# Kernel optimization log

Measured on AMD Instinct MI355X. Metric: run time of the kernel, lower is better.

## Reference

```python
import jax, jax.numpy as jnp
import numpy as np

KX, KZ = 3, 3          # heterogeneity_x, heterogeneity_z
DX, DZ, DU = 3, 3, 3   # depths
LX, LZ = 16, 16        # last_x, last_z
TOL = 1e-6


def setup_inputs() -> dict:
    key = jax.random.key(0)
    ks = jax.random.split(key, 11)
    B, n, dx, dz = 8192, 50, 32, 20
    WXw, WZw, WUw = 64, 64, 128

    def w(k, shape):
        return jax.random.normal(k, shape, jnp.float32) * (1.0 / np.sqrt(shape[-2]))

    return {
        "X": jax.random.normal(ks[0], (B, n, dx), jnp.float32),
        "Z": jax.random.normal(ks[1], (B, dz), jnp.float32),
        "Wx0": w(ks[2], (KX, dx, WXw)),
        "Wx": w(ks[3], (KX, DX - 1, WXw, WXw)),
        "Wlx": w(ks[4], (KX, WXw, LX)),
        "Wz0": w(ks[5], (KZ, dz, WZw)),
        "Wz": w(ks[6], (KZ, DZ - 1, WZw, WZw)),
        "Wlz": w(ks[7], (KZ, WZw, LZ)),
        "Wu0": w(ks[8], (dx + LX + LZ + dz, WUw)),
        "Wu": w(ks[9], (DU - 1, WUw, WUw)),
        "Wlast": w(ks[10], (WUw, 1)),
    }


def reference(X, Z, Wx0, Wx, Wlx, Wz0, Wz, Wlz, Wu0, Wu, Wlast):
    B, n, dx = X.shape
    dz = Z.shape[-1]

    # --- product-feature MLP per heterogeneity i, batched over all n products ---
    # NOTE (faithful to original bug): the leaked loop var `k` means
    # last_x[DX-1] is used for EVERY heterogeneity index i.
    def x_branch(w0, wh):
        h = jax.nn.elu(jnp.einsum('bnd,dw->bnw', X, w0))
        for k in range(wh.shape[0]):
            h = jax.nn.elu(jnp.einsum('bnw,wv->bnv', h, wh[k]))
        return jnp.einsum('bnw,wl->bnl', h, Wlx[DX - 1])  # linear last layer

    Xi = jax.vmap(x_branch)(Wx0, Wx)  # [KX, B, n, LX]

    # --- customer-feature MLP per heterogeneity j ---
    def z_branch(w0, wh, wl):
        h = jax.nn.elu(Z @ w0)
        for k in range(wh.shape[0]):
            h = jax.nn.elu(h @ wh[k])
        return h @ wl  # linear last layer

    Zj = jax.vmap(z_branch)(Wz0, Wz, Wlz)  # [KZ, B, LZ]

    # --- utility MLP over all (i, j) heterogeneity pairs; average of softmaxes ---
    acc = jnp.zeros((B, n), X.dtype)
    for i in range(KX):
        for j in range(KZ):
            zb = jnp.broadcast_to(Zj[j][:, None, :], (B, n, LZ))
            zu = jnp.broadcast_to(Z[:, None, :], (B, n, dz))
            u = jnp.concatenate([X, Xi[i], zb, zu], axis=-1)  # [B, n, dx+LX+LZ+dz]
            u = jax.nn.elu(u @ Wu0)
            for k in range(Wu.shape[0]):
                u = jax.nn.elu(u @ Wu[k])
            score = (u @ Wlast)[..., 0]  # [B, n]
            acc = acc + (TOL + jax.nn.softmax(score, axis=-1)) / (1.0 + TOL * n)
    return acc / (KX * KZ)
```

## Files before the change

### kernel.cpp

```cpp
#include <hip/hip_runtime.h>
#include <math.h>

#define NPROD 50
#define DXF 32
#define DZF 20
#define WUW 128
#define LXD 16
#define LZD 16

typedef __attribute__((ext_vector_type(8))) short short8;
typedef __attribute__((ext_vector_type(4))) float float4_;

__device__ __forceinline__ short f2bf(float x) {
    unsigned u = __builtin_bit_cast(unsigned, x);
    u += 0x7fffu + ((u >> 16) & 1u);
    return (short)(u >> 16);
}
__device__ __forceinline__ unsigned pkbf(float a, float b) {
#if __has_builtin(__builtin_amdgcn_cvt_pk_bf16_f32)
    auto v = __builtin_amdgcn_cvt_pk_bf16_f32(a, b);
    return __builtin_bit_cast(unsigned, v);
#else
    return (unsigned)(unsigned short)f2bf(a) | ((unsigned)(unsigned short)f2bf(b) << 16);
#endif
}
__device__ __forceinline__ float elu_med3(float x) {
    float e = __builtin_amdgcn_exp2f(x * 1.44269504089f) - 1.0f;
#if __has_builtin(__builtin_amdgcn_fmed3f)
    return __builtin_amdgcn_fmed3f(x, e, 0.0f);
#else
    return x > 0.0f ? x : e;
#endif
}
__device__ __forceinline__ float elu_fast(float x) {
    float e = __builtin_amdgcn_exp2f(x * 1.44269504089f) - 1.0f;
    return x > 0.0f ? x : e;
}
#define MFMA16(a, b, c) __builtin_amdgcn_mfma_f32_16x16x32_bf16((a), (b), (c), 0, 0, 0)

#define PK_WX0   0
#define PK_WX    6144
#define PK_WLX2  30720
#define PK_WU0   31744
#define PK_WU    39936
#define PK_WLAST 72704
#define PK_TOTAL 74752
#define NB_PACK  292
#define WS_NEEDED ((size_t)PK_TOTAL * 2)

__device__ __forceinline__ short* su_ptr(short* buf, int row, int chunk) {
    return buf + (row << 7) + ((chunk ^ (row & 15)) << 3);
}
__device__ __forceinline__ const short* su_ptr(const short* buf, int row, int chunk) {
    return buf + (row << 7) + ((chunk ^ (row & 15)) << 3);
}
__device__ __forceinline__ short* sa_ptr(short* buf, int row, int chunk) {
    return buf + (row << 6) + ((chunk ^ (row & 7)) << 3);
}
__device__ __forceinline__ const short* sa_ptr(const short* buf, int row, int chunk) {
    return buf + (row << 6) + ((chunk ^ (row & 7)) << 3);
}

template<bool ACT>
__device__ __forceinline__ void epi_store(short* chunk_base, int half, float4_ a) {
    float e0, e1, e2, e3;
    if (ACT) { e0 = elu_med3(a[0]); e1 = elu_med3(a[1]); e2 = elu_med3(a[2]); e3 = elu_med3(a[3]); }
    else { e0 = a[0]; e1 = a[1]; e2 = a[2]; e3 = a[3]; }
    uint2 p; p.x = pkbf(e0, e1); p.y = pkbf(e2, e3);
    *(uint2*)(chunk_base + half * 4) = p;
}

__global__ void pack_weights(const float* __restrict__ Wx0, const float* __restrict__ Wx,
                             const float* __restrict__ Wlx, const float* __restrict__ Wu0,
                             const float* __restrict__ Wu, const float* __restrict__ Wlast,
                             short* __restrict__ pk)
{
    int idx = blockIdx.x * 256 + threadIdx.x;
    if (idx >= PK_TOTAL) return;
    float v;
    if (idx < PK_WX) {
        int m = idx / 2048, r = idx % 2048, n = r / 32, k = r % 32;
        v = Wx0[m * 2048 + k * 64 + n];
    } else if (idx < PK_WLX2) {
        int t = idx - PK_WX; int m = t / 4096, r = t % 4096, n = r / 64, k = r % 64;
        v = Wx[m * 4096 + k * 64 + n];
    } else if (idx < PK_WU0) {
        int r = idx - PK_WLX2; int n = r / 64, k = r % 64;
        v = Wlx[2 * 1024 + k * 16 + n];
    } else if (idx < PK_WU) {
        int r = idx - PK_WU0; int n = r / 64, k = r % 64;
        v = (k < 48) ? Wu0[k * 128 + n] : 0.0f;
    } else if (idx < PK_WLAST) {
        int t = idx - PK_WU; int m = t / 16384, r = t % 16384, n = r / 128, k = r % 128;
        v = Wu[m * 16384 + k * 128 + n];
    } else {
        int r = idx - PK_WLAST; int n = r / 128, k = r % 128;
        v = (n == 0) ? Wlast[k] : 0.0f;
    }
    pk[idx] = f2bf(v);
}

__global__ __launch_bounds__(256, 3) void rum_main(
    const float* __restrict__ X, const float* __restrict__ Z,
    const float* __restrict__ Wz0, const float* __restrict__ Wz,
    const float* __restrict__ Wlz, const float* __restrict__ Wu0,
    const short* __restrict__ pk, float* __restrict__ out)
{
    __shared__ __align__(16) short sA0[64 * 64];
    __shared__ __align__(16) short sU[64 * 128];
    __shared__ __align__(16) float sPreZ[3 * 128];
    __shared__ float sScore[2][64];
    __shared__ float sZb[DZF];
    __shared__ float zA[3][64], zB[3][64];
    __shared__ float sZj[3][LZD];

    const int tid = threadIdx.x;
    const int w = tid >> 6, lane = tid & 63;
    const int quad = lane >> 4, l15 = lane & 15;
    const long b = blockIdx.x;
    const short8 zero8 = (short8)0;

    for (int it = tid; it < 100; it += 256) {
        int r = it >> 1, ch = 6 + (it & 1);
        *(short8*)sa_ptr(sA0, r, ch) = zero8;
    }
    if (tid < 112) {
        int r = 50 + (tid >> 3), ch = tid & 7;
        *(short8*)sa_ptr(sA0, r, ch) = zero8;
    }
    for (int it = tid; it < 400; it += 256) {
        int r = it >> 3, c4 = it & 7;
        float4_ xv = *(const float4_*)(X + (b * 50 + r) * 32 + c4 * 4);
        uint2 p; p.x = pkbf(xv[0], xv[1]); p.y = pkbf(xv[2], xv[3]);
        *(uint2*)(sa_ptr(sA0, r, c4 >> 1) + (c4 & 1) * 4) = p;
    }
    if (tid < DZF) sZb[tid] = Z[b * DZF + tid];
    __syncthreads();

    if (w < 3) {
        const float* wv = Wz0 + w * (DZF * 64);
        float s0 = 0.f, s1 = 0.f;
        #pragma unroll
        for (int k = 0; k < DZF; k += 2) {
            s0 = fmaf(sZb[k], wv[k * 64 + lane], s0);
            s1 = fmaf(sZb[k + 1], wv[(k + 1) * 64 + lane], s1);
        }
        zA[w][lane] = elu_fast(s0 + s1);
    }
    __syncthreads();
    if (w < 3) {
        const float* wv = Wz + (w * 2 + 0) * 4096;
        float s0 = 0.f, s1 = 0.f;
        #pragma unroll
        for (int k = 0; k < 64; k += 2) {
            s0 = fmaf(zA[w][k], wv[k * 64 + lane], s0);
            s1 = fmaf(zA[w][k + 1], wv[(k + 1) * 64 + lane], s1);
        }
        zB[w][lane] = elu_fast(s0 + s1);
    }
    __syncthreads();
    if (w < 3) {
        const float* wv = Wz + (w * 2 + 1) * 4096;
        float s0 = 0.f, s1 = 0.f;
        #pragma unroll
        for (int k = 0; k < 64; k += 2) {
            s0 = fmaf(zB[w][k], wv[k * 64 + lane], s0);
            s1 = fmaf(zB[w][k + 1], wv[(k + 1) * 64 + lane], s1);
        }
        zA[w][lane] = elu_fast(s0 + s1);
    }
    __syncthreads();
    if (w < 3 && lane < LZD) {
        const float* wv = Wlz + w * (64 * LZD);
        float s0 = 0.f, s1 = 0.f;
        #pragma unroll
        for (int k = 0; k < 64; k += 2) {
            s0 = fmaf(zA[w][k], wv[k * LZD + lane], s0);
            s1 = fmaf(zA[w][k + 1], wv[(k + 1) * LZD + lane], s1);
        }
        sZj[w][lane] = s0 + s1;
    }
    __syncthreads();
    if (w < 3) {
        #pragma unroll
        for (int half = 0; half < 2; ++half) {
            const int c = lane + half * 64;
            float s = 0.f;
            #pragma unroll
            for (int k = 0; k < LZD; ++k) s = fmaf(sZj[w][k], Wu0[(48 + k) * WUW + c], s);
            #pragma unroll
            for (int k = 0; k < DZF; ++k) s = fmaf(sZb[k], Wu0[(64 + k) * WUW + c], s);
            sPreZ[w * 128 + c] = s;
        }
    }
    __syncthreads();

    float accv = 0.f;
    const float inv_norm = 1.0f / (1.0f + 1e-6f * (float)NPROD);

    for (int i = 0; i < 3; ++i) {
        {
            const short* A = pk + PK_WX0 + i * 2048;
            short8 af = *(const short8*)(A + (w * 16 + l15) * 32 + quad * 8);
            #pragma unroll
            for (int pt = 0; pt < 4; ++pt) {
                short8 bfr = *(const short8*)sa_ptr(sA0, pt * 16 + l15, quad);
                float4_ acc = MFMA16(af, bfr, (float4_)0.f);
                epi_store<true>(su_ptr(sU, pt * 16 + l15, 2 * w + (quad >> 1)), quad & 1, acc);
            }
        }
        __syncthreads();
        for (int l = 0; l < 2; ++l) {
            const short* A = pk + PK_WX + (i * 2 + l) * 4096;
            short8 af0 = *(const short8*)(A + (w * 16 + l15) * 64 + quad * 8);
            short8 af1 = *(const short8*)(A + (w * 16 + l15) * 64 + 32 + quad * 8);
            float4_ accx[4];
            #pragma unroll
            for (int pt = 0; pt < 4; ++pt) {
                short8 b0 = *(const short8*)su_ptr(sU, pt * 16 + l15, quad);
                short8 b1 = *(const short8*)su_ptr(sU, pt * 16 + l15, 4 + quad);
                accx[pt] = MFMA16(af0, b0, (float4_)0.f);
                accx[pt] = MFMA16(af1, b1, accx[pt]);
            }
            __syncthreads();
            #pragma unroll
            for (int pt = 0; pt < 4; ++pt)
                epi_store<true>(su_ptr(sU, pt * 16 + l15, 2 * w + (quad >> 1)), quad & 1, accx[pt]);
            __syncthreads();
        }
        {
            const short* A = pk + PK_WLX2;
            short8 af0 = *(const short8*)(A + l15 * 64 + quad * 8);
            short8 af1 = *(const short8*)(A + l15 * 64 + 32 + quad * 8);
            short8 b0 = *(const short8*)su_ptr(sU, w * 16 + l15, quad);
            short8 b1 = *(const short8*)su_ptr(sU, w * 16 + l15, 4 + quad);
            float4_ acc = MFMA16(af0, b0, (float4_)0.f);
            acc = MFMA16(af1, b1, acc);
            epi_store<false>(sa_ptr(sA0, w * 16 + l15, 4 + (quad >> 1)), quad & 1, acc);
        }
        __syncthreads();

        for (int j = 0; j < 3; ++j) {
            const int pass = i * 3 + j;
            {
                const short* A = pk + PK_WU0;
                #pragma unroll
                for (int wi = 0; wi < 2; ++wi) {
                    const int wt = w * 2 + wi;
                    float4_ pz = *(const float4_*)(sPreZ + j * 128 + wt * 16 + quad * 4);
                    short8 af0 = *(const short8*)(A + (wt * 16 + l15) * 64 + quad * 8);
                    short8 af1 = *(const short8*)(A + (wt * 16 + l15) * 64 + 32 + quad * 8);
                    #pragma unroll
                    for (int pt = 0; pt < 4; ++pt) {
                        short8 b0 = *(const short8*)sa_ptr(sA0, pt * 16 + l15, quad);
                        short8 b1 = *(const short8*)sa_ptr(sA0, pt * 16 + l15, 4 + quad);
                        float4_ t = MFMA16(af0, b0, pz);
                        t = MFMA16(af1, b1, t);
                        epi_store<true>(su_ptr(sU, pt * 16 + l15, 2 * wt + (quad >> 1)), quad & 1, t);
                    }
                }
            }
            __syncthreads();

            for (int l = 0; l < 2; ++l) {
                const short* A = pk + PK_WU + l * 16384;
                float4_ ad[2][4];
                #pragma unroll
                for (int wi = 0; wi < 2; ++wi)
                    #pragma unroll
                    for (int pt = 0; pt < 4; ++pt) ad[wi][pt] = (float4_)0.f;
                #pragma unroll
                for (int ks = 0; ks < 4; ++ks) {
                    short8 bf[4];
                    #pragma unroll
                    for (int pt = 0; pt < 4; ++pt)
                        bf[pt] = *(const short8*)su_ptr(sU, pt * 16 + l15, ks * 4 + quad);
                    #pragma unroll
                    for (int wi = 0; wi < 2; ++wi) {
                        short8 af = *(const short8*)(A + ((w * 2 + wi) * 16 + l15) * 128 + ks * 32 + quad * 8);
                        #pragma unroll
                        for (int pt = 0; pt < 4; ++pt)
                            ad[wi][pt] = MFMA16(af, bf[pt], ad[wi][pt]);
                    }
                }
                __syncthreads();
                #pragma unroll
                for (int wi = 0; wi < 2; ++wi)
                    #pragma unroll
                    for (int pt = 0; pt < 4; ++pt)
                        epi_store<true>(su_ptr(sU, pt * 16 + l15, 2 * (w * 2 + wi) + (quad >> 1)),
                                        quad & 1, ad[wi][pt]);
                __syncthreads();
            }

            {
                const short* A = pk + PK_WLAST;
                float4_ as = (float4_)0.f;
                #pragma unroll
                for (int ks = 0; ks < 4; ++ks) {
                    short8 af = *(const short8*)(A + l15 * 128 + ks * 32 + quad * 8);
                    short8 bf = *(const short8*)su_ptr(sU, w * 16 + l15, ks * 4 + quad);
                    as = MFMA16(af, bf, as);
                }
                if (quad == 0) sScore[pass & 1][w * 16 + l15] = as[0];
            }
            __syncthreads();
            if (tid < 64) {
                float sc = (tid < NPROD) ? sScore[pass & 1][tid] : -3.0e38f;
                float m = sc;
                #pragma unroll
                for (int off = 32; off > 0; off >>= 1) m = fmaxf(m, __shfl_xor(m, off));
                float e = (tid < NPROD) ? __builtin_amdgcn_exp2f((sc - m) * 1.44269504089f) : 0.f;
                float ssum = e;
                #pragma unroll
                for (int off = 32; off > 0; off >>= 1) ssum += __shfl_xor(ssum, off);
                if (tid < NPROD) accv += (1e-6f + e / ssum) * inv_norm;
            }
        }
    }
    if (tid < NPROD) out[b * 50 + tid] = accv * (1.0f / 9.0f);
}

__device__ __forceinline__ float elu_f(float x) { return x > 0.0f ? x : expm1f(x); }
template<int IN, int OUT, bool ACT>
__device__ __forceinline__ void dense50(const float* __restrict__ in_lds,
                                        const float* __restrict__ Wg,
                                        float* __restrict__ out_lds)
{
    const int tid = threadIdx.x;
    constexpr int CQ = OUT / 4;
    const float4* __restrict__ W4 = (const float4*)Wg;
    for (int item = tid; item < 25 * CQ; item += 256) {
        const int rp = item / CQ, cq = item % CQ;
        const int r0 = rp, r1 = rp + 25;
        float4 a0 = {0,0,0,0}, a1 = {0,0,0,0};
        for (int k = 0; k < IN; ++k) {
            const float4 wv = W4[k * CQ + cq];
            const float x0 = in_lds[r0 * IN + k], x1 = in_lds[r1 * IN + k];
            a0.x = fmaf(x0, wv.x, a0.x); a0.y = fmaf(x0, wv.y, a0.y);
            a0.z = fmaf(x0, wv.z, a0.z); a0.w = fmaf(x0, wv.w, a0.w);
            a1.x = fmaf(x1, wv.x, a1.x); a1.y = fmaf(x1, wv.y, a1.y);
            a1.z = fmaf(x1, wv.z, a1.z); a1.w = fmaf(x1, wv.w, a1.w);
        }
        if (ACT) {
            a0.x = elu_f(a0.x); a0.y = elu_f(a0.y); a0.z = elu_f(a0.z); a0.w = elu_f(a0.w);
            a1.x = elu_f(a1.x); a1.y = elu_f(a1.y); a1.z = elu_f(a1.z); a1.w = elu_f(a1.w);
        }
        ((float4*)out_lds)[r0 * CQ + cq] = a0;
        ((float4*)out_lds)[r1 * CQ + cq] = a1;
    }
}
template<bool ACT>
__device__ __forceinline__ void dense128fb(const float* __restrict__ in_lds,
                                           const float* __restrict__ Wg,
                                           float* __restrict__ out_lds)
{
    const int tid = threadIdx.x;
    const float4* __restrict__ W4 = (const float4*)Wg;
    for (int item = tid; item < 13 * 32; item += 256) {
        const int rg = item >> 5, cq = item & 31;
        int r[4];
        #pragma unroll
        for (int t = 0; t < 4; ++t) r[t] = min(rg * 4 + t, NPROD - 1);
        float4 a[4];
        #pragma unroll
        for (int t = 0; t < 4; ++t) a[t] = make_float4(0, 0, 0, 0);
        for (int k = 0; k < 128; ++k) {
            const float4 wv = W4[k * 32 + cq];
            #pragma unroll
            for (int t = 0; t < 4; ++t) {
                const float x = in_lds[r[t] * 128 + k];
                a[t].x = fmaf(x, wv.x, a[t].x); a[t].y = fmaf(x, wv.y, a[t].y);
                a[t].z = fmaf(x, wv.z, a[t].z); a[t].w = fmaf(x, wv.w, a[t].w);
            }
        }
        #pragma unroll
        for (int t = 0; t < 4; ++t) {
            const int row = rg * 4 + t;
            if (row < NPROD) {
                float4 o = a[t];
                if (ACT) { o.x = elu_f(o.x); o.y = elu_f(o.y); o.z = elu_f(o.z); o.w = elu_f(o.w); }
                ((float4*)out_lds)[row * 32 + cq] = o;
            }
        }
    }
}
__device__ __forceinline__ void dense_u0fb(const float* __restrict__ sXb,
                                           const float* __restrict__ sXi,
                                           const float* __restrict__ preZ_j,
                                           const float* __restrict__ Wu0,
                                           float* __restrict__ out_lds)
{
    const int tid = threadIdx.x;
    const float4* __restrict__ W4 = (const float4*)Wu0;
    const float4* __restrict__ PZ4 = (const float4*)preZ_j;
    for (int item = tid; item < 13 * 32; item += 256) {
        const int rg = item >> 5, cq = item & 31;
        int r[4];
        #pragma unroll
        for (int t = 0; t < 4; ++t) r[t] = min(rg * 4 + t, NPROD - 1);
        const float4 pz = PZ4[cq];
        float4 a[4];
        #pragma unroll
        for (int t = 0; t < 4; ++t) a[t] = pz;
        for (int k = 0; k < DXF; ++k) {
            const float4 wv = W4[k * 32 + cq];
            #pragma unroll
            for (int t = 0; t < 4; ++t) {
                const float x = sXb[r[t] * DXF + k];
                a[t].x = fmaf(x, wv.x, a[t].x); a[t].y = fmaf(x, wv.y, a[t].y);
                a[t].z = fmaf(x, wv.z, a[t].z); a[t].w = fmaf(x, wv.w, a[t].w);
            }
        }
        for (int k = 0; k < LXD; ++k) {
            const float4 wv = W4[(DXF + k) * 32 + cq];
            #pragma unroll
            for (int t = 0; t < 4; ++t) {
                const float x = sXi[r[t] * LXD + k];
                a[t].x = fmaf(x, wv.x, a[t].x); a[t].y = fmaf(x, wv.y, a[t].y);
                a[t].z = fmaf(x, wv.z, a[t].z); a[t].w = fmaf(x, wv.w, a[t].w);
            }
        }
        #pragma unroll
        for (int t = 0; t < 4; ++t) {
            const int row = rg * 4 + t;
            if (row < NPROD) {
                float4 o = a[t];
                o.x = elu_f(o.x); o.y = elu_f(o.y); o.z = elu_f(o.z); o.w = elu_f(o.w);
                ((float4*)out_lds)[row * 32 + cq] = o;
            }
        }
    }
}
__global__ __launch_bounds__(256, 2) void rum_fused_fb(
    const float* __restrict__ X, const float* __restrict__ Z,
    const float* __restrict__ Wx0, const float* __restrict__ Wx,
    const float* __restrict__ Wlx, const float* __restrict__ Wz0,
    const float* __restrict__ Wz, const float* __restrict__ Wlz,
    const float* __restrict__ Wu0, const float* __restrict__ Wu,
    const float* __restrict__ Wlast, float* __restrict__ out)
{
    __shared__ __align__(16) float sBufA[NPROD * WUW];
    __shared__ __align__(16) float sBufB[NPROD * WUW];
    __shared__ __align__(16) float sXb[NPROD * DXF];
    __shared__ __align__(16) float sXi[NPROD * LXD];
    __shared__ __align__(16) float sPreZ[3 * WUW];
    const int b = blockIdx.x, tid = threadIdx.x;
    float* zsm = sBufA; float* zh0 = sBufA + 64; float* zh1 = sBufA + 256; float* zjd = sBufA + 448;
    {
        const float* Xg = X + (size_t)b * (NPROD * DXF);
        for (int idx = tid; idx < NPROD * DXF; idx += 256) sXb[idx] = Xg[idx];
        const float* Zg = Z + (size_t)b * DZF;
        if (tid < DZF) zsm[tid] = Zg[tid];
    }
    __syncthreads();
    const int zj = tid >> 6, zc = tid & 63;
    if (zj < 3) { const float* wv = Wz0 + zj * (DZF * 64); float s = 0;
        for (int k = 0; k < DZF; ++k) s = fmaf(zsm[k], wv[k * 64 + zc], s);
        zh0[zj * 64 + zc] = elu_f(s); }
    __syncthreads();
    if (zj < 3) { const float* wv = Wz + (zj * 2 + 0) * 4096; float s = 0;
        for (int k = 0; k < 64; ++k) s = fmaf(zh0[zj * 64 + k], wv[k * 64 + zc], s);
        zh1[zj * 64 + zc] = elu_f(s); }
    __syncthreads();
    if (zj < 3) { const float* wv = Wz + (zj * 2 + 1) * 4096; float s = 0;
        for (int k = 0; k < 64; ++k) s = fmaf(zh1[zj * 64 + k], wv[k * 64 + zc], s);
        zh0[zj * 64 + zc] = elu_f(s); }
    __syncthreads();
    if (tid < 48) { const int j = tid >> 4, c = tid & 15;
        const float* wv = Wlz + j * (64 * LZD); float s = 0;
        for (int k = 0; k < 64; ++k) s = fmaf(zh0[j * 64 + k], wv[k * LZD + c], s);
        zjd[j * LZD + c] = s; }
    __syncthreads();
    for (int idx = tid; idx < 3 * WUW; idx += 256) {
        const int j = idx >> 7, c = idx & 127; float s = 0;
        for (int k = 0; k < LZD; ++k) s = fmaf(zjd[j * LZD + k], Wu0[(DXF + LXD + k) * WUW + c], s);
        for (int k = 0; k < DZF; ++k) s = fmaf(zsm[k], Wu0[(DXF + LXD + LZD + k) * WUW + c], s);
        sPreZ[idx] = s;
    }
    __syncthreads();
    float accv = 0.f;
    const float inv_norm = 1.0f / (1.0f + 1e-6f * (float)NPROD);
    for (int i = 0; i < 3; ++i) {
        dense50<DXF, 64, true>(sXb, Wx0 + i * (DXF * 64), sBufA); __syncthreads();
        dense50<64, 64, true>(sBufA, Wx + (i * 2 + 0) * 4096, sBufB); __syncthreads();
        dense50<64, 64, true>(sBufB, Wx + (i * 2 + 1) * 4096, sBufA); __syncthreads();
        dense50<64, LXD, false>(sBufA, Wlx + 2 * (64 * LXD), sXi); __syncthreads();
        for (int j = 0; j < 3; ++j) {
            dense_u0fb(sXb, sXi, sPreZ + j * WUW, Wu0, sBufA); __syncthreads();
            dense128fb<true>(sBufA, Wu, sBufB); __syncthreads();
            dense128fb<true>(sBufB, Wu + 16384, sBufA); __syncthreads();
            if (tid < 64) {
                float sc = -3.0e38f;
                if (tid < NPROD) { float s = 0;
                    for (int k = 0; k < WUW; ++k) s = fmaf(sBufA[tid * WUW + k], Wlast[k], s);
                    sc = s; }
                float m = sc;
                #pragma unroll
                for (int off = 32; off > 0; off >>= 1) m = fmaxf(m, __shfl_xor(m, off));
                float e = (tid < NPROD) ? expf(sc - m) : 0.f;
                float ssum = e;
                #pragma unroll
                for (int off = 32; off > 0; off >>= 1) ssum += __shfl_xor(ssum, off);
                if (tid < NPROD) accv += (1e-6f + e / ssum) * inv_norm;
            }
            __syncthreads();
        }
    }
    if (tid < NPROD) out[(size_t)b * NPROD + tid] = accv * (1.0f / 9.0f);
}

extern "C" void kernel_launch(void* const* d_in, const int* in_sizes, int n_in,
                              void* d_out, int out_size, void* d_ws, size_t ws_size,
                              hipStream_t stream) {
    const float* X     = (const float*)d_in[0];
    const float* Z     = (const float*)d_in[1];
    const float* Wx0   = (const float*)d_in[2];
    const float* Wx    = (const float*)d_in[3];
    const float* Wlx   = (const float*)d_in[4];
    const float* Wz0   = (const float*)d_in[5];
    const float* Wz    = (const float*)d_in[6];
    const float* Wlz   = (const float*)d_in[7];
    const float* Wu0   = (const float*)d_in[8];
    const float* Wu    = (const float*)d_in[9];
    const float* Wlast = (const float*)d_in[10];
    float* out = (float*)d_out;

    if (ws_size < WS_NEEDED) {
        rum_fused_fb<<<dim3(8192), dim3(256), 0, stream>>>(
            X, Z, Wx0, Wx, Wlx, Wz0, Wz, Wlz, Wu0, Wu, Wlast, out);
        return;
    }

    short* pk = (short*)d_ws;
    pack_weights<<<dim3(NB_PACK), dim3(256), 0, stream>>>(
        Wx0, Wx, Wlx, Wu0, Wu, Wlast, pk);
    rum_main<<<dim3(8192), dim3(256), 0, stream>>>(
        X, Z, Wz0, Wz, Wlz, Wu0, pk, out);
}
```

Before: 933.5 us.

## Raise occupancy to four blocks per CU by cutting registers and shared memory

Raises the launch bound from three to four blocks per CU. To fit, the Z-branch scratch arrays now alias the sU buffer instead of taking their own shared memory. The X-branch hidden layers ping-pong between the two halves of sU, which drops one barrier per layer. The wide utility layers compute the two output tiles one after the other, packing the first into bf16 before the second, so fewer fp32 accumulators are live. The cost is reloading the B fragments twice from LDS, with some risk of spills under the tighter register budget.

```diff
diff --git a/kernel.cpp b/kernel.cpp
--- a/kernel.cpp
+++ b/kernel.cpp
@@ -53,6 +53,12 @@
 }
 __device__ __forceinline__ const short* su_ptr(const short* buf, int row, int chunk) {
     return buf + (row << 7) + ((chunk ^ (row & 15)) << 3);
+}
+__device__ __forceinline__ short* sx_ptr(short* buf, int h, int row, int chunk) {
+    return buf + (row << 7) + (h << 6) + ((chunk ^ (row & 7)) << 3);
+}
+__device__ __forceinline__ const short* sx_ptr(const short* buf, int h, int row, int chunk) {
+    return buf + (row << 7) + (h << 6) + ((chunk ^ (row & 7)) << 3);
 }
 __device__ __forceinline__ short* sa_ptr(short* buf, int row, int chunk) {
     return buf + (row << 6) + ((chunk ^ (row & 7)) << 3);
@@ -100,7 +106,7 @@
     pk[idx] = f2bf(v);
 }
 
-__global__ __launch_bounds__(256, 3) void rum_main(
+__global__ __launch_bounds__(256, 4) void rum_main(
     const float* __restrict__ X, const float* __restrict__ Z,
     const float* __restrict__ Wz0, const float* __restrict__ Wz,
     const float* __restrict__ Wlz, const float* __restrict__ Wu0,
@@ -110,9 +116,12 @@
     __shared__ __align__(16) short sU[64 * 128];
     __shared__ __align__(16) float sPreZ[3 * 128];
     __shared__ float sScore[2][64];
-    __shared__ float sZb[DZF];
-    __shared__ float zA[3][64], zB[3][64];
-    __shared__ float sZj[3][LZD];
+
+    float* zs  = (float*)sU;
+    float* zA  = zs;
+    float* zB  = zs + 192;
+    float* zZj = zs + 384;
+    float* zZb = zs + 432;
 
     const int tid = threadIdx.x;
     const int w = tid >> 6, lane = tid & 63;
@@ -134,7 +143,7 @@
         uint2 p; p.x = pkbf(xv[0], xv[1]); p.y = pkbf(xv[2], xv[3]);
         *(uint2*)(sa_ptr(sA0, r, c4 >> 1) + (c4 & 1) * 4) = p;
     }
-    if (tid < DZF) sZb[tid] = Z[b * DZF + tid];
+    if (tid < DZF) zZb[tid] = Z[b * DZF + tid];
     __syncthreads();
 
     if (w < 3) {
@@ -142,10 +151,10 @@
         float s0 = 0.f, s1 = 0.f;
         #pragma unroll
         for (int k = 0; k < DZF; k += 2) {
-            s0 = fmaf(sZb[k], wv[k * 64 + lane], s0);
-            s1 = fmaf(sZb[k + 1], wv[(k + 1) * 64 + lane], s1);
-        }
-        zA[w][lane] = elu_fast(s0 + s1);
+            s0 = fmaf(zZb[k], wv[k * 64 + lane], s0);
+            s1 = fmaf(zZb[k + 1], wv[(k + 1) * 64 + lane], s1);
+        }
+        zA[w * 64 + lane] = elu_fast(s0 + s1);
     }
     __syncthreads();
     if (w < 3) {
@@ -153,10 +162,10 @@
         float s0 = 0.f, s1 = 0.f;
         #pragma unroll
         for (int k = 0; k < 64; k += 2) {
-            s0 = fmaf(zA[w][k], wv[k * 64 + lane], s0);
-            s1 = fmaf(zA[w][k + 1], wv[(k + 1) * 64 + lane], s1);
-        }
-        zB[w][lane] = elu_fast(s0 + s1);
+            s0 = fmaf(zA[w * 64 + k], wv[k * 64 + lane], s0);
+            s1 = fmaf(zA[w * 64 + k + 1], wv[(k + 1) * 64 + lane], s1);
+        }
+        zB[w * 64 + lane] = elu_fast(s0 + s1);
     }
     __syncthreads();
     if (w < 3) {
@@ -164,10 +173,10 @@
         float s0 = 0.f, s1 = 0.f;
         #pragma unroll
         for (int k = 0; k < 64; k += 2) {
-            s0 = fmaf(zB[w][k], wv[k * 64 + lane], s0);
-            s1 = fmaf(zB[w][k + 1], wv[(k + 1) * 64 + lane], s1);
-        }
-        zA[w][lane] = elu_fast(s0 + s1);
+            s0 = fmaf(zB[w * 64 + k], wv[k * 64 + lane], s0);
+            s1 = fmaf(zB[w * 64 + k + 1], wv[(k + 1) * 64 + lane], s1);
+        }
+        zA[w * 64 + lane] = elu_fast(s0 + s1);
     }
     __syncthreads();
     if (w < 3 && lane < LZD) {
@@ -175,10 +184,10 @@
         float s0 = 0.f, s1 = 0.f;
         #pragma unroll
         for (int k = 0; k < 64; k += 2) {
-            s0 = fmaf(zA[w][k], wv[k * LZD + lane], s0);
-            s1 = fmaf(zA[w][k + 1], wv[(k + 1) * LZD + lane], s1);
-        }
-        sZj[w][lane] = s0 + s1;
+            s0 = fmaf(zA[w * 64 + k], wv[k * LZD + lane], s0);
+            s1 = fmaf(zA[w * 64 + k + 1], wv[(k + 1) * LZD + lane], s1);
+        }
+        zZj[w * LZD + lane] = s0 + s1;
     }
     __syncthreads();
     if (w < 3) {
@@ -187,9 +196,9 @@
             const int c = lane + half * 64;
             float s = 0.f;
             #pragma unroll
-            for (int k = 0; k < LZD; ++k) s = fmaf(sZj[w][k], Wu0[(48 + k) * WUW + c], s);
-            #pragma unroll
-            for (int k = 0; k < DZF; ++k) s = fmaf(sZb[k], Wu0[(64 + k) * WUW + c], s);
+            for (int k = 0; k < LZD; ++k) s = fmaf(zZj[w * LZD + k], Wu0[(48 + k) * WUW + c], s);
+            #pragma unroll
+            for (int k = 0; k < DZF; ++k) s = fmaf(zZb[k], Wu0[(64 + k) * WUW + c], s);
             sPreZ[w * 128 + c] = s;
         }
     }
@@ -206,34 +215,31 @@
             for (int pt = 0; pt < 4; ++pt) {
                 short8 bfr = *(const short8*)sa_ptr(sA0, pt * 16 + l15, quad);
                 float4_ acc = MFMA16(af, bfr, (float4_)0.f);
-                epi_store<true>(su_ptr(sU, pt * 16 + l15, 2 * w + (quad >> 1)), quad & 1, acc);
+                epi_store<true>(sx_ptr(sU, 0, pt * 16 + l15, 2 * w + (quad >> 1)), quad & 1, acc);
             }
         }
         __syncthreads();
         for (int l = 0; l < 2; ++l) {
             const short* A = pk + PK_WX + (i * 2 + l) * 4096;
+            const int hin = l, hout = 1 - l;
             short8 af0 = *(const short8*)(A + (w * 16 + l15) * 64 + quad * 8);
             short8 af1 = *(const short8*)(A + (w * 16 + l15) * 64 + 32 + quad * 8);
-            float4_ accx[4];
             #pragma unroll
             for (int pt = 0; pt < 4; ++pt) {
-                short8 b0 = *(const short8*)su_ptr(sU, pt * 16 + l15, quad);
-                short8 b1 = *(const short8*)su_ptr(sU, pt * 16 + l15, 4 + quad);
-                accx[pt] = MFMA16(af0, b0, (float4_)0.f);
-                accx[pt] = MFMA16(af1, b1, accx[pt]);
-            }
-            __syncthreads();
-            #pragma unroll
-            for (int pt = 0; pt < 4; ++pt)
-                epi_store<true>(su_ptr(sU, pt * 16 + l15, 2 * w + (quad >> 1)), quad & 1, accx[pt]);
+                short8 b0 = *(const short8*)sx_ptr(sU, hin, pt * 16 + l15, quad);
+                short8 b1 = *(const short8*)sx_ptr(sU, hin, pt * 16 + l15, 4 + quad);
+                float4_ acc = MFMA16(af0, b0, (float4_)0.f);
+                acc = MFMA16(af1, b1, acc);
+                epi_store<true>(sx_ptr(sU, hout, pt * 16 + l15, 2 * w + (quad >> 1)), quad & 1, acc);
+            }
             __syncthreads();
         }
         {
             const short* A = pk + PK_WLX2;
             short8 af0 = *(const short8*)(A + l15 * 64 + quad * 8);
             short8 af1 = *(const short8*)(A + l15 * 64 + 32 + quad * 8);
-            short8 b0 = *(const short8*)su_ptr(sU, w * 16 + l15, quad);
-            short8 b1 = *(const short8*)su_ptr(sU, w * 16 + l15, 4 + quad);
+            short8 b0 = *(const short8*)sx_ptr(sU, 0, w * 16 + l15, quad);
+            short8 b1 = *(const short8*)sx_ptr(sU, 0, w * 16 + l15, 4 + quad);
             float4_ acc = MFMA16(af0, b0, (float4_)0.f);
             acc = MFMA16(af1, b1, acc);
             epi_store<false>(sa_ptr(sA0, w * 16 + l15, 4 + (quad >> 1)), quad & 1, acc);
@@ -264,32 +270,45 @@
 
             for (int l = 0; l < 2; ++l) {
                 const short* A = pk + PK_WU + l * 16384;
-                float4_ ad[2][4];
-                #pragma unroll
-                for (int wi = 0; wi < 2; ++wi)
+                uint2 p0[4];
+                {
+                    float4_ ac[4];
                     #pragma unroll
-                    for (int pt = 0; pt < 4; ++pt) ad[wi][pt] = (float4_)0.f;
+                    for (int pt = 0; pt < 4; ++pt) ac[pt] = (float4_)0.f;
+                    #pragma unroll
+                    for (int ks = 0; ks < 4; ++ks) {
+                        short8 af = *(const short8*)(A + ((w * 2 + 0) * 16 + l15) * 128 + ks * 32 + quad * 8);
+                        #pragma unroll
+                        for (int pt = 0; pt < 4; ++pt) {
+                            short8 bf = *(const short8*)su_ptr(sU, pt * 16 + l15, ks * 4 + quad);
+                            ac[pt] = MFMA16(af, bf, ac[pt]);
+                        }
+                    }
+                    #pragma unroll
+                    for (int pt = 0; pt < 4; ++pt) {
+                        p0[pt].x = pkbf(elu_med3(ac[pt][0]), elu_med3(ac[pt][1]));
+                        p0[pt].y = pkbf(elu_med3(ac[pt][2]), elu_med3(ac[pt][3]));
+                    }
+                }
+                float4_ ac1[4];
+                #pragma unroll
+                for (int pt = 0; pt < 4; ++pt) ac1[pt] = (float4_)0.f;
                 #pragma unroll
                 for (int ks = 0; ks < 4; ++ks) {
-                    short8 bf[4];
+                    short8 af = *(const short8*)(A + ((w * 2 + 1) * 16 + l15) * 128 + ks * 32 + quad * 8);
                     #pragma unroll
-                    for (int pt = 0; pt < 4; ++pt)
-                        bf[pt] = *(const short8*)su_ptr(sU, pt * 16 + l15, ks * 4 + quad);
-                    #pragma unroll
-                    for (int wi = 0; wi < 2; ++wi) {
-                        short8 af = *(const short8*)(A + ((w * 2 + wi) * 16 + l15) * 128 + ks * 32 + quad * 8);
-                        #pragma unroll
-                        for (int pt = 0; pt < 4; ++pt)
-                            ad[wi][pt] = MFMA16(af, bf[pt], ad[wi][pt]);
+                    for (int pt = 0; pt < 4; ++pt) {
+                        short8 bf = *(const short8*)su_ptr(sU, pt * 16 + l15, ks * 4 + quad);
+                        ac1[pt] = MFMA16(af, bf, ac1[pt]);
                     }
                 }
                 __syncthreads();
                 #pragma unroll
-                for (int wi = 0; wi < 2; ++wi)
-                    #pragma unroll
-                    for (int pt = 0; pt < 4; ++pt)
-                        epi_store<true>(su_ptr(sU, pt * 16 + l15, 2 * (w * 2 + wi) + (quad >> 1)),
-                                        quad & 1, ad[wi][pt]);
+                for (int pt = 0; pt < 4; ++pt)
+                    *(uint2*)(su_ptr(sU, pt * 16 + l15, 2 * (w * 2 + 0) + (quad >> 1)) + (quad & 1) * 4) = p0[pt];
+                #pragma unroll
+                for (int pt = 0; pt < 4; ++pt)
+                    epi_store<true>(su_ptr(sU, pt * 16 + l15, 2 * (w * 2 + 1) + (quad >> 1)), quad & 1, ac1[pt]);
                 __syncthreads();
             }
 
```

Measured after the change: 1.148 ms. +23.0%, slower.
